# Kernel tuning notes

Hardware: AMD Instinct MI355X
Metric: run time of the kernel (lower is better)

## Reference

```python
import jax, jax.numpy as jnp
from jax import lax
import numpy as np


def _lstm_layer(x, Wih, Whh, bih, bhh):
    """Single-direction LSTM layer, PyTorch gate order (i, f, g, o).
    x: [B, T, D_in] -> hidden sequence [B, T, H]."""
    B, T, _ = x.shape
    H = Whh.shape[1]
    # Precompute input contribution for all timesteps: [B, T, 4H]
    xw = jnp.einsum('btd,gd->btg', x, Wih) + bih + bhh

    def step(carry, xt):
        h, c = carry
        gates = xt + h @ Whh.T  # [B, 4H]
        i, f, g, o = jnp.split(gates, 4, axis=-1)
        i = jax.nn.sigmoid(i)
        f = jax.nn.sigmoid(f)
        g = jnp.tanh(g)
        o = jax.nn.sigmoid(o)
        c = f * c + i * g
        h = o * jnp.tanh(c)
        return (h, c), h

    h0 = jnp.zeros((B, H), dtype=x.dtype)
    c0 = jnp.zeros((B, H), dtype=x.dtype)
    _, hs = lax.scan(step, (h0, c0), jnp.swapaxes(xw, 0, 1))  # [T, B, H]
    return jnp.swapaxes(hs, 0, 1)  # [B, T, H]


def setup_inputs() -> dict:
    key = jax.random.key(0)
    ks = jax.random.split(key, 9)
    B, T, D, H = 64, 2048, 256, 128
    s = 1.0 / np.sqrt(H)  # PyTorch uniform(-1/sqrt(H), 1/sqrt(H)) init scale
    u = lambda k, shp: jax.random.uniform(k, shp, jnp.float32, -s, s)
    return {
        'x': jax.random.normal(ks[0], (B, T, D), jnp.float32),
        'Wih0': u(ks[1], (4 * H, D)),
        'Whh0': u(ks[2], (4 * H, H)),
        'bih0': u(ks[3], (4 * H,)),
        'bhh0': u(ks[4], (4 * H,)),
        'Wih1': u(ks[5], (4 * H, H)),
        'Whh1': u(ks[6], (4 * H, H)),
        'bih1': u(ks[7], (4 * H,)),
        'bhh1': u(ks[8], (4 * H,)),
    }


def reference(x, Wih0, Whh0, bih0, bhh0, Wih1, Whh1, bih1, bhh1):
    # 2-layer stacked LSTM; inter-layer dropout (p=0.1) is identity at eval.
    h1 = _lstm_layer(x, Wih0, Whh0, bih0, bhh0)
    h2 = _lstm_layer(h1, Wih1, Whh1, bih1, bhh1)
    return h2
```

## Files before the change

kernel.cpp:

```cpp
#include <hip/hip_runtime.h>
#include <hip/hip_bf16.h>

#define H 128
#define FOURH 512
#define BATCH 64
#define SEQ 2048
#define TC SEQ
#define NCHUNK 128
#define GSTRIDE (BATCH * FOURH)

typedef _Float16 half8 __attribute__((ext_vector_type(8)));
typedef float f32x4 __attribute__((ext_vector_type(4)));

__global__ void prep_kernel(const float* __restrict__ Wih0,
                            const float* __restrict__ bih0, const float* __restrict__ bhh0,
                            const float* __restrict__ bih1, const float* __restrict__ bhh1,
                            const float* __restrict__ Wih1,
                            float* __restrict__ Wt0,
                            float* __restrict__ b0, float* __restrict__ b1,
                            _Float16* __restrict__ wt1h,
                            int* __restrict__ flags) {
    int id = blockIdx.x * 256 + threadIdx.x;
    const int N0 = 256 * 512;
    if (id < N0) {
        int k = id >> 9, n = id & 511;
        Wt0[id] = Wih0[n * 256 + k];
    } else if (id < N0 + 512) {
        int i = id - N0;
        b0[i] = bih0[i] + bhh0[i];
    } else if (id < N0 + 1024) {
        int i = id - (N0 + 512);
        b1[i] = bih1[i] + bhh1[i];
    } else if (id < N0 + 1024 + 65536) {
        int i = id - (N0 + 1024);
        wt1h[i] = (_Float16)Wih1[i];
    } else if (id < N0 + 1024 + 65536 + 272) {
        flags[id - (N0 + 1024 + 65536)] = 0;
    }
}

__device__ __forceinline__ float sigmoid_f(float x) {
    return __builtin_amdgcn_rcpf(1.f + __expf(-x));
}
__device__ __forceinline__ float tanh_f(float x) {
    return 1.f - 2.f * __builtin_amdgcn_rcpf(__expf(2.f * x) + 1.f);
}

#define LDS_BARRIER()                                                \
    do {                                                             \
        asm volatile("s_waitcnt lgkmcnt(0)" ::: "memory");           \
        __builtin_amdgcn_s_barrier();                                \
        __builtin_amdgcn_sched_barrier(0);                           \
    } while (0)

#define BM 128
#define BN 128
#define BK 32

__global__ __launch_bounds__(512, 2) void lstm_fused_kernel(
    const float* __restrict__ x,
    const float* __restrict__ Wt0,
    const float* __restrict__ b0sum,
    float* __restrict__ Gbuf,
    const float* __restrict__ Whh0,
    const _Float16* __restrict__ wt1h,
    const float* __restrict__ Whh1,
    const float* __restrict__ b1,
    _Float16* __restrict__ h1p,
    float* __restrict__ out,
    int* __restrict__ flags)
{
    const int tid = threadIdx.x;

    int* prodF     = flags;
    int* chunkDone = flags + 16;
    int* g1Done    = flags + 144;

    __shared__ _Float16 hbuf[2][8][136];
    __shared__ float As[BK][BM + 4];
    __shared__ float Bs[BK][BN];

    if (blockIdx.x >= 176) {
        const int j   = blockIdx.x - 176;
        const int sub = j & 31;
        const int cls = j >> 5;
        const int by  = sub >> 2;
        const int bx  = sub & 3;
        const int n0  = bx * BN;
        const int wv  = tid >> 6;
        const int l   = tid & 63;
        const int li  = l & 15;
        const int q   = l >> 4;
        const int gb1 = 8 * by + wv;

        float bv1g[8];
#pragma unroll
        for (int ct = 0; ct < 8; ++ct) bv1g[ct] = b1[n0 + ct * 16 + li];

        for (int m = cls; m < NCHUNK; m += 2) {
            if (tid == 0) {
                while (__hip_atomic_load(&prodF[by], __ATOMIC_RELAXED,
                                         __HIP_MEMORY_SCOPE_AGENT) < 16 * (m + 1))
                    __builtin_amdgcn_s_sleep(4);
                (void)__hip_atomic_load(&prodF[by], __ATOMIC_ACQUIRE,
                                        __HIP_MEMORY_SCOPE_AGENT);
            }
            __syncthreads();

            const int t0 = m * 16;
            half8 Af[4];
            const _Float16* ap = h1p + ((size_t)(t0 + li) * BATCH + gb1) * H + q * 8;
#pragma unroll
            for (int kf = 0; kf < 4; ++kf)
                Af[kf] = *(const half8*)(ap + kf * 32);

            f32x4 acc1[8];
#pragma unroll
            for (int ct = 0; ct < 8; ++ct) {
                acc1[ct][0] = bv1g[ct]; acc1[ct][1] = bv1g[ct];
                acc1[ct][2] = bv1g[ct]; acc1[ct][3] = bv1g[ct];
            }
#pragma unroll
            for (int ct = 0; ct < 8; ++ct) {
                const _Float16* wp = wt1h + (size_t)(n0 + ct * 16 + li) * H + q * 8;
#pragma unroll
                for (int kf = 0; kf < 4; ++kf) {
                    half8 Bfr = *(const half8*)(wp + kf * 32);
                    acc1[ct] = __builtin_amdgcn_mfma_f32_16x16x32_f16(Af[kf], Bfr, acc1[ct], 0, 0, 0);
                }
            }
            const int srow = t0 + q * 4;
#pragma unroll
            for (int ct = 0; ct < 8; ++ct)
#pragma unroll
                for (int i = 0; i < 4; ++i)
                    Gbuf[((size_t)(srow + i) * BATCH + gb1) * FOURH + n0 + ct * 16 + li] = acc1[ct][i];
            __syncthreads();
            if (tid == 0) {
                __threadfence();
                __hip_atomic_fetch_add(&g1Done[m], 1, __ATOMIC_RELEASE,
                                       __HIP_MEMORY_SCOPE_AGENT);
            }
        }
        return;
    }

    if (blockIdx.x >= 16) {
        const int j   = blockIdx.x - 16;
        const int sub = j & 31;
        const int cls = j >> 5;
        const int by  = sub >> 2;
        const int bx  = sub & 3;
        const int n0  = bx * BN;
        const int tm  = tid >> 5;
        const int tn  = tid & 31;

        int ar[2], aq[2], bkk[2], bq[2];
#pragma unroll
        for (int l2 = 0; l2 < 2; ++l2) {
            int fidx = tid + l2 * 512;
            ar[l2] = fidx >> 3; aq[l2] = fidx & 7;
            bkk[l2] = fidx >> 5; bq[l2] = fidx & 31;
        }
        float4 bvg = *(const float4*)&b0sum[n0 + tn * 4];

        for (int idx = cls; idx < NCHUNK; idx += 5) {
            const float* aptr[2];
#pragma unroll
            for (int l2 = 0; l2 < 2; ++l2) {
                int rl = by * BM + ar[l2];
                int b = rl >> 4;
                int t = idx * 16 + (rl & 15);
                aptr[l2] = x + ((size_t)b * SEQ + t) * 256 + aq[l2] * 4;
            }
            float acc[2][4][4];
#pragma unroll
            for (int rh = 0; rh < 2; ++rh)
#pragma unroll
                for (int i = 0; i < 4; ++i)
#pragma unroll
                    for (int jj = 0; jj < 4; ++jj) acc[rh][i][jj] = 0.f;

            for (int k0 = 0; k0 < 256; k0 += BK) {
                __syncthreads();
#pragma unroll
                for (int l2 = 0; l2 < 2; ++l2) {
                    float4 v = *(const float4*)(aptr[l2] + k0);
                    As[aq[l2] * 4 + 0][ar[l2]] = v.x;
                    As[aq[l2] * 4 + 1][ar[l2]] = v.y;
                    As[aq[l2] * 4 + 2][ar[l2]] = v.z;
                    As[aq[l2] * 4 + 3][ar[l2]] = v.w;
                }
#pragma unroll
                for (int l2 = 0; l2 < 2; ++l2) {
                    float4 v = *(const float4*)(Wt0 + (size_t)(k0 + bkk[l2]) * FOURH + n0 + bq[l2] * 4);
                    *(float4*)&Bs[bkk[l2]][bq[l2] * 4] = v;
                }
                __syncthreads();
#pragma unroll
                for (int kk = 0; kk < BK; ++kk) {
                    float a[8], bb[4];
                    *(float4*)&a[0] = *(const float4*)&As[kk][tm * 4];
                    *(float4*)&a[4] = *(const float4*)&As[kk][64 + tm * 4];
                    *(float4*)&bb[0] = *(const float4*)&Bs[kk][tn * 4];
#pragma unroll
                    for (int rh = 0; rh < 2; ++rh)
#pragma unroll
                        for (int i = 0; i < 4; ++i)
#pragma unroll
                            for (int jj = 0; jj < 4; ++jj)
                                acc[rh][i][jj] = fmaf(a[rh * 4 + i], bb[jj], acc[rh][i][jj]);
                }
            }
#pragma unroll
            for (int rh = 0; rh < 2; ++rh)
#pragma unroll
                for (int i = 0; i < 4; ++i) {
                    int rl = by * BM + rh * 64 + tm * 4 + i;
                    int b = rl >> 4;
                    int t = idx * 16 + (rl & 15);
                    float* gp = Gbuf + ((size_t)t * BATCH + b) * FOURH + n0 + tn * 4;
                    float4 o = make_float4(acc[rh][i][0] + bvg.x, acc[rh][i][1] + bvg.y,
                                           acc[rh][i][2] + bvg.z, acc[rh][i][3] + bvg.w);
                    *(float4*)gp = o;
                }
            __syncthreads();
            if (tid == 0) {
                __threadfence();
                __hip_atomic_fetch_add(&chunkDone[idx], 1, __ATOMIC_RELEASE,
                                       __HIP_MEMORY_SCOPE_AGENT);
            }
        }
        return;
    }

    const int w  = tid >> 6;
    const int l  = tid & 63;
    const int li = l & 15;
    const int q  = l >> 4;
    const int u  = 16 * w + li;
    const int b0 = q * 2;
    const int ab = ((li >> 2) * 2) + (li & 1);

#define WAIT_FLAG(ptr, tgtv)                                                   \
    do {                                                                       \
        if (tid == 0) {                                                        \
            while (__hip_atomic_load((ptr), __ATOMIC_RELAXED,                  \
                                     __HIP_MEMORY_SCOPE_AGENT) < (tgtv))       \
                __builtin_amdgcn_s_sleep(4);                                   \
            (void)__hip_atomic_load((ptr), __ATOMIC_ACQUIRE,                   \
                                    __HIP_MEMORY_SCOPE_AGENT);                 \
        }                                                                      \
        __syncthreads();                                                       \
    } while (0)

#define SCAN_STEP(S, PB, GR, BFARR, STORE_STMT)                                   \
    {                                                                             \
        half8 Afr[4];                                                             \
        _Pragma("unroll")                                                         \
        for (int kf = 0; kf < 4; ++kf)                                            \
            Afr[kf] = *(const half8*)&hbuf[PB][ab][kf * 32 + q * 8];              \
        f32x4 acc[4];                                                             \
        _Pragma("unroll")                                                         \
        for (int tl = 0; tl < 4; ++tl) {                                          \
            acc[tl][0] = GR[tl * 2 + 0]; acc[tl][1] = GR[tl * 2 + 1];             \
            acc[tl][2] = 0.f;            acc[tl][3] = 0.f;                        \
        }                                                                         \
        {                                                                         \
            int sl_ = (S) + 4; if (sl_ > TC - 1) sl_ = TC - 1;                    \
            const float* gp_ = Gbuf + (size_t)sl_ * GSTRIDE;                      \
            _Pragma("unroll")                                                     \
            for (int tl = 0; tl < 4; ++tl) {                                      \
                GR[tl * 2 + 0] = gp_[boff0 + tl * H];                             \
                GR[tl * 2 + 1] = gp_[boff1 + tl * H];                             \
            }                                                                     \
        }                                                                         \
        _Pragma("unroll")                                                         \
        for (int kf = 0; kf < 4; ++kf)                                            \
            _Pragma("unroll")                                                     \
            for (int tl = 0; tl < 4; ++tl)                                        \
                acc[tl] = __builtin_amdgcn_mfma_f32_16x16x32_f16(Afr[kf], BFARR[tl][kf], acc[tl], 0, 0, 0); \
        {                                                                         \
            float ig = sigmoid_f(acc[0][0]);                                      \
            float fg = sigmoid_f(acc[1][0]);                                      \
            float gg = tanh_f(acc[2][0]);                                         \
            float og = sigmoid_f(acc[3][0]);                                      \
            c0 = fmaf(fg, c0, ig * gg);                                           \
            h0 = og * tanh_f(c0);                                                 \
            float ig1 = sigmoid_f(acc[0][1]);                                     \
            float fg1 = sigmoid_f(acc[1][1]);                                     \
            float gg1 = tanh_f(acc[2][1]);                                        \
            float og1 = sigmoid_f(acc[3][1]);                                     \
            c1 = fmaf(fg1, c1, ig1 * gg1);                                        \
            h1v = og1 * tanh_f(c1);                                               \
        }                                                                         \
        hbuf[PB ^ 1][b0][u]     = (_Float16)h0;                                   \
        hbuf[PB ^ 1][b0 + 1][u] = (_Float16)h1v;                                  \
        STORE_STMT                                                                \
        LDS_BARRIER();                                                            \
    }

    const int g = (blockIdx.x < 8) ? blockIdx.x : blockIdx.x - 8;
    const int boff0 = (8 * g + b0) * FOURH + u;
    const int boff1 = boff0 + FOURH;

    if (blockIdx.x < 8) {
        half8 Bf[4][4];
#pragma unroll
        for (int tl = 0; tl < 4; ++tl)
#pragma unroll
            for (int kf = 0; kf < 4; ++kf) {
                const float* wp = Whh0 + (size_t)(tl * 128 + u) * H + kf * 32 + q * 8;
                float4 v0 = *(const float4*)wp;
                float4 v1 = *(const float4*)(wp + 4);
                half8 b;
                b[0] = (_Float16)v0.x; b[1] = (_Float16)v0.y;
                b[2] = (_Float16)v0.z; b[3] = (_Float16)v0.w;
                b[4] = (_Float16)v1.x; b[5] = (_Float16)v1.y;
                b[6] = (_Float16)v1.z; b[7] = (_Float16)v1.w;
                Bf[tl][kf] = b;
            }

        float c0 = 0.f, c1 = 0.f, h0 = 0.f, h1v = 0.f;
        hbuf[0][b0][u]     = (_Float16)0.f;
        hbuf[0][b0 + 1][u] = (_Float16)0.f;

        WAIT_FLAG(&chunkDone[0], 32);

        float Ga[8], Gb[8], Gc[8], Gd[8];
#pragma unroll
        for (int tl = 0; tl < 4; ++tl) {
            Ga[tl * 2 + 0] = Gbuf[(size_t)0 * GSTRIDE + boff0 + tl * H];
            Ga[tl * 2 + 1] = Gbuf[(size_t)0 * GSTRIDE + boff1 + tl * H];
            Gb[tl * 2 + 0] = Gbuf[(size_t)1 * GSTRIDE + boff0 + tl * H];
            Gb[tl * 2 + 1] = Gbuf[(size_t)1 * GSTRIDE + boff1 + tl * H];
            Gc[tl * 2 + 0] = Gbuf[(size_t)2 * GSTRIDE + boff0 + tl * H];
            Gc[tl * 2 + 1] = Gbuf[(size_t)2 * GSTRIDE + boff1 + tl * H];
            Gd[tl * 2 + 0] = Gbuf[(size_t)3 * GSTRIDE + boff0 + tl * H];
            Gd[tl * 2 + 1] = Gbuf[(size_t)3 * GSTRIDE + boff1 + tl * H];
        }

        _Float16* php = h1p + (size_t)(8 * g + b0) * H + u;

#define P_STORE { php[0] = (_Float16)h0; php[128] = (_Float16)h1v; php += BATCH * H; }

        for (int s4 = 0; s4 < TC; s4 += 4) {
            if ((s4 & 15) == 0) {
                int k = (s4 >> 4) + 1;
                if (k > NCHUNK - 1) k = NCHUNK - 1;
                WAIT_FLAG(&chunkDone[k], 32);
            }
            SCAN_STEP(s4 + 0, 0, Ga, Bf, P_STORE)
            SCAN_STEP(s4 + 1, 1, Gb, Bf, P_STORE)
            SCAN_STEP(s4 + 2, 0, Gc, Bf, P_STORE)
            SCAN_STEP(s4 + 3, 1, Gd, Bf, P_STORE)
            if ((s4 & 15) == 12) {
                __threadfence();
                __syncthreads();
                if (tid == 0)
                    __hip_atomic_store(&prodF[g], s4 + 4, __ATOMIC_RELEASE,
                                       __HIP_MEMORY_SCOPE_AGENT);
            }
        }
#undef P_STORE
    } else {
        half8 Bf[4][4];
#pragma unroll
        for (int tl = 0; tl < 4; ++tl)
#pragma unroll
            for (int kf = 0; kf < 4; ++kf) {
                const float* wp = Whh1 + (size_t)(tl * 128 + u) * H + kf * 32 + q * 8;
                float4 v0 = *(const float4*)wp;
                float4 v1 = *(const float4*)(wp + 4);
                half8 b;
                b[0] = (_Float16)v0.x; b[1] = (_Float16)v0.y;
                b[2] = (_Float16)v0.z; b[3] = (_Float16)v0.w;
                b[4] = (_Float16)v1.x; b[5] = (_Float16)v1.y;
                b[6] = (_Float16)v1.z; b[7] = (_Float16)v1.w;
                Bf[tl][kf] = b;
            }

        float c0 = 0.f, c1 = 0.f, h0, h1v;
        hbuf[0][b0][u]     = (_Float16)0.f;
        hbuf[0][b0 + 1][u] = (_Float16)0.f;

        float* op0 = out + (size_t)(8 * g + b0) * SEQ * H + u;
        float* op1 = out + (size_t)(8 * g + b0 + 1) * SEQ * H + u;

        WAIT_FLAG(&prodF[g], 96);
        WAIT_FLAG(&g1Done[0], 32);

        float Ga[8], Gb[8], Gc[8], Gd[8];
#pragma unroll
        for (int tl = 0; tl < 4; ++tl) {
            Ga[tl * 2 + 0] = Gbuf[(size_t)0 * GSTRIDE + boff0 + tl * H];
            Ga[tl * 2 + 1] = Gbuf[(size_t)0 * GSTRIDE + boff1 + tl * H];
            Gb[tl * 2 + 0] = Gbuf[(size_t)1 * GSTRIDE + boff0 + tl * H];
            Gb[tl * 2 + 1] = Gbuf[(size_t)1 * GSTRIDE + boff1 + tl * H];
            Gc[tl * 2 + 0] = Gbuf[(size_t)2 * GSTRIDE + boff0 + tl * H];
            Gc[tl * 2 + 1] = Gbuf[(size_t)2 * GSTRIDE + boff1 + tl * H];
            Gd[tl * 2 + 0] = Gbuf[(size_t)3 * GSTRIDE + boff0 + tl * H];
            Gd[tl * 2 + 1] = Gbuf[(size_t)3 * GSTRIDE + boff1 + tl * H];
        }

#define C_STORE { op0[0] = h0; op1[0] = h1v; op0 += H; op1 += H; }

        for (int s4 = 0; s4 < TC; s4 += 4) {
            if ((s4 & 15) == 0) {
                int k = (s4 >> 4) + 1;
                if (k > NCHUNK - 1) k = NCHUNK - 1;
                WAIT_FLAG(&g1Done[k], 32);
            }
            SCAN_STEP(s4 + 0, 0, Ga, Bf, C_STORE)
            SCAN_STEP(s4 + 1, 1, Gb, Bf, C_STORE)
            SCAN_STEP(s4 + 2, 0, Gc, Bf, C_STORE)
            SCAN_STEP(s4 + 3, 1, Gd, Bf, C_STORE)
        }
#undef C_STORE
    }
#undef WAIT_FLAG
#undef SCAN_STEP
}

extern "C" void kernel_launch(void* const* d_in, const int* in_sizes, int n_in,
                              void* d_out, int out_size, void* d_ws, size_t ws_size,
                              hipStream_t stream) {
    const float* x    = (const float*)d_in[0];
    const float* Wih0 = (const float*)d_in[1];
    const float* Whh0 = (const float*)d_in[2];
    const float* bih0 = (const float*)d_in[3];
    const float* bhh0 = (const float*)d_in[4];
    const float* Wih1 = (const float*)d_in[5];
    const float* Whh1 = (const float*)d_in[6];
    const float* bih1 = (const float*)d_in[7];
    const float* bhh1 = (const float*)d_in[8];
    float* out = (float*)d_out;

    char* ws = (char*)d_ws;
    size_t off = 0;
    auto carve = [&](size_t bytes) -> char* {
        char* p = ws + off;
        off += (bytes + 255) & ~(size_t)255;
        return p;
    };

    float*     Wt0   = (float*)carve(256 * 512 * 4);
    float*     b0v   = (float*)carve(512 * 4);
    float*     b1v   = (float*)carve(512 * 4);
    _Float16*  wt1h  = (_Float16*)carve(65536 * 2);
    _Float16*  h1p   = (_Float16*)carve((size_t)SEQ * BATCH * H * 2);
    int*       flags = (int*)carve(272 * 4);
    float*     gbuf  = (float*)carve((size_t)SEQ * GSTRIDE * 4);

    prep_kernel<<<774, 256, 0, stream>>>(Wih0, bih0, bhh0, bih1, bhh1, Wih1,
                                         Wt0, b0v, b1v, wt1h, flags);

    lstm_fused_kernel<<<240, 512, 0, stream>>>(x, Wt0, b0v, gbuf,
                                               Whh0, wt1h, Whh1, b1v,
                                               h1p, out, flags);
}
```

Before: 2.498 ms.

## Move layer-0 input projection GEMM into a separate kernel before fused scan

Layer-0's input-projection GEMM no longer runs inside the persistent fused kernel as 160 producer blocks. It now runs as a standalone tiled FP32 GEMM kernel with bias, launched before the fused LSTM kernel, which shrinks to 80 blocks. The chunkDone flag waits in the layer-0 scan are dropped, so that scan reads precomputed gates directly. This removes the flag polling and the LDS/register pressure the GEMM blocks added to the persistent kernel. In exchange, the GEMM no longer overlaps with the serial recurrence, so its full time is added before the scan starts.

```diff
diff --git a/kernel.cpp b/kernel.cpp
--- a/kernel.cpp
+++ b/kernel.cpp
@@ -39,6 +39,108 @@
     }
 }
 
+#define BM 128
+#define BN 128
+#define BK 32
+
+__global__ __launch_bounds__(256) void gemm_bias_kernel(
+    const float* __restrict__ A, int lda, int rowsPerBatch, int t0,
+    const float* __restrict__ Bt, const float* __restrict__ bias,
+    float* __restrict__ G, int K, int tcShift)
+{
+    __shared__ float As[BK][BM + 4];
+    __shared__ float Bs[BK][BN];
+
+    const int tid = threadIdx.x;
+    const int m0 = blockIdx.y * BM;
+    const int n0 = blockIdx.x * BN;
+    const int tm = tid >> 4;
+    const int tn = tid & 15;
+    const int tcMask = (1 << tcShift) - 1;
+
+    const float* aptr[4];
+    int ar[4], aq[4];
+#pragma unroll
+    for (int l = 0; l < 4; ++l) {
+        int fidx = tid + l * 256;
+        int r = fidx >> 3, q = fidx & 7;
+        ar[l] = r; aq[l] = q;
+        int m = m0 + r;
+        int bi = m >> tcShift;
+        int tl = m & tcMask;
+        aptr[l] = A + ((size_t)bi * rowsPerBatch + t0 + tl) * lda + q * 4;
+    }
+    int bkk[4], bq[4];
+#pragma unroll
+    for (int l = 0; l < 4; ++l) {
+        int fidx = tid + l * 256;
+        bkk[l] = fidx >> 5; bq[l] = fidx & 31;
+    }
+
+    float acc[2][2][4][4];
+#pragma unroll
+    for (int ri = 0; ri < 2; ++ri)
+#pragma unroll
+        for (int ci = 0; ci < 2; ++ci)
+#pragma unroll
+            for (int i = 0; i < 4; ++i)
+#pragma unroll
+                for (int j = 0; j < 4; ++j) acc[ri][ci][i][j] = 0.f;
+
+    for (int k0 = 0; k0 < K; k0 += BK) {
+        __syncthreads();
+#pragma unroll
+        for (int l = 0; l < 4; ++l) {
+            float4 v = *(const float4*)(aptr[l] + k0);
+            As[aq[l] * 4 + 0][ar[l]] = v.x;
+            As[aq[l] * 4 + 1][ar[l]] = v.y;
+            As[aq[l] * 4 + 2][ar[l]] = v.z;
+            As[aq[l] * 4 + 3][ar[l]] = v.w;
+        }
+#pragma unroll
+        for (int l = 0; l < 4; ++l) {
+            float4 v = *(const float4*)(Bt + (size_t)(k0 + bkk[l]) * FOURH + n0 + bq[l] * 4);
+            *(float4*)&Bs[bkk[l]][bq[l] * 4] = v;
+        }
+        __syncthreads();
+#pragma unroll
+        for (int kk = 0; kk < BK; ++kk) {
+            float a[8], bb[8];
+            *(float4*)&a[0] = *(const float4*)&As[kk][tm * 4];
+            *(float4*)&a[4] = *(const float4*)&As[kk][64 + tm * 4];
+            *(float4*)&bb[0] = *(const float4*)&Bs[kk][tn * 4];
+            *(float4*)&bb[4] = *(const float4*)&Bs[kk][64 + tn * 4];
+#pragma unroll
+            for (int ri = 0; ri < 2; ++ri)
+#pragma unroll
+                for (int i = 0; i < 4; ++i)
+#pragma unroll
+                    for (int ci = 0; ci < 2; ++ci)
+#pragma unroll
+                        for (int j = 0; j < 4; ++j)
+                            acc[ri][ci][i][j] = fmaf(a[ri * 4 + i], bb[ci * 4 + j], acc[ri][ci][i][j]);
+        }
+    }
+
+    float4 bv0 = *(const float4*)&bias[n0 + tn * 4];
+    float4 bv1 = *(const float4*)&bias[n0 + 64 + tn * 4];
+#pragma unroll
+    for (int ri = 0; ri < 2; ++ri)
+#pragma unroll
+        for (int i = 0; i < 4; ++i) {
+            int m = m0 + ri * 64 + tm * 4 + i;
+            int bi = m >> tcShift;
+            int tl = m & tcMask;
+            float* gp = G + ((size_t)tl * BATCH + bi) * FOURH + n0;
+            float4 o0 = make_float4(acc[ri][0][i][0] + bv0.x, acc[ri][0][i][1] + bv0.y,
+                                    acc[ri][0][i][2] + bv0.z, acc[ri][0][i][3] + bv0.w);
+            float4 o1 = make_float4(acc[ri][1][i][0] + bv1.x, acc[ri][1][i][1] + bv1.y,
+                                    acc[ri][1][i][2] + bv1.z, acc[ri][1][i][3] + bv1.w);
+            *(float4*)(gp + tn * 4) = o0;
+            *(float4*)(gp + 64 + tn * 4) = o1;
+        }
+}
+
 __device__ __forceinline__ float sigmoid_f(float x) {
     return __builtin_amdgcn_rcpf(1.f + __expf(-x));
 }
@@ -53,14 +155,7 @@
         __builtin_amdgcn_sched_barrier(0);                           \
     } while (0)
 
-#define BM 128
-#define BN 128
-#define BK 32
-
 __global__ __launch_bounds__(512, 2) void lstm_fused_kernel(
-    const float* __restrict__ x,
-    const float* __restrict__ Wt0,
-    const float* __restrict__ b0sum,
     float* __restrict__ Gbuf,
     const float* __restrict__ Whh0,
     const _Float16* __restrict__ wt1h,
@@ -72,21 +167,18 @@
 {
     const int tid = threadIdx.x;
 
-    int* prodF     = flags;
-    int* chunkDone = flags + 16;
-    int* g1Done    = flags + 144;
+    int* prodF  = flags;
+    int* g1Done = flags + 144;
 
     __shared__ _Float16 hbuf[2][8][136];
-    __shared__ float As[BK][BM + 4];
-    __shared__ float Bs[BK][BN];
-
-    if (blockIdx.x >= 176) {
-        const int j   = blockIdx.x - 176;
+
+    if (blockIdx.x >= 16) {
+        const int j   = blockIdx.x - 16;
         const int sub = j & 31;
         const int cls = j >> 5;
         const int by  = sub >> 2;
         const int bx  = sub & 3;
-        const int n0  = bx * BN;
+        const int n0  = bx * 128;
         const int wv  = tid >> 6;
         const int l   = tid & 63;
         const int li  = l & 15;
@@ -139,95 +231,6 @@
             if (tid == 0) {
                 __threadfence();
                 __hip_atomic_fetch_add(&g1Done[m], 1, __ATOMIC_RELEASE,
-                                       __HIP_MEMORY_SCOPE_AGENT);
-            }
-        }
-        return;
-    }
-
-    if (blockIdx.x >= 16) {
-        const int j   = blockIdx.x - 16;
-        const int sub = j & 31;
-        const int cls = j >> 5;
-        const int by  = sub >> 2;
-        const int bx  = sub & 3;
-        const int n0  = bx * BN;
-        const int tm  = tid >> 5;
-        const int tn  = tid & 31;
-
-        int ar[2], aq[2], bkk[2], bq[2];
-#pragma unroll
-        for (int l2 = 0; l2 < 2; ++l2) {
-            int fidx = tid + l2 * 512;
-            ar[l2] = fidx >> 3; aq[l2] = fidx & 7;
-            bkk[l2] = fidx >> 5; bq[l2] = fidx & 31;
-        }
-        float4 bvg = *(const float4*)&b0sum[n0 + tn * 4];
-
-        for (int idx = cls; idx < NCHUNK; idx += 5) {
-            const float* aptr[2];
-#pragma unroll
-            for (int l2 = 0; l2 < 2; ++l2) {
-                int rl = by * BM + ar[l2];
-                int b = rl >> 4;
-                int t = idx * 16 + (rl & 15);
-                aptr[l2] = x + ((size_t)b * SEQ + t) * 256 + aq[l2] * 4;
-            }
-            float acc[2][4][4];
-#pragma unroll
-            for (int rh = 0; rh < 2; ++rh)
-#pragma unroll
-                for (int i = 0; i < 4; ++i)
-#pragma unroll
-                    for (int jj = 0; jj < 4; ++jj) acc[rh][i][jj] = 0.f;
-
-            for (int k0 = 0; k0 < 256; k0 += BK) {
-                __syncthreads();
-#pragma unroll
-                for (int l2 = 0; l2 < 2; ++l2) {
-                    float4 v = *(const float4*)(aptr[l2] + k0);
-                    As[aq[l2] * 4 + 0][ar[l2]] = v.x;
-                    As[aq[l2] * 4 + 1][ar[l2]] = v.y;
-                    As[aq[l2] * 4 + 2][ar[l2]] = v.z;
-                    As[aq[l2] * 4 + 3][ar[l2]] = v.w;
-                }
-#pragma unroll
-                for (int l2 = 0; l2 < 2; ++l2) {
-                    float4 v = *(const float4*)(Wt0 + (size_t)(k0 + bkk[l2]) * FOURH + n0 + bq[l2] * 4);
-                    *(float4*)&Bs[bkk[l2]][bq[l2] * 4] = v;
-                }
-                __syncthreads();
-#pragma unroll
-                for (int kk = 0; kk < BK; ++kk) {
-                    float a[8], bb[4];
-                    *(float4*)&a[0] = *(const float4*)&As[kk][tm * 4];
-                    *(float4*)&a[4] = *(const float4*)&As[kk][64 + tm * 4];
-                    *(float4*)&bb[0] = *(const float4*)&Bs[kk][tn * 4];
-#pragma unroll
-                    for (int rh = 0; rh < 2; ++rh)
-#pragma unroll
-                        for (int i = 0; i < 4; ++i)
-#pragma unroll
-                            for (int jj = 0; jj < 4; ++jj)
-                                acc[rh][i][jj] = fmaf(a[rh * 4 + i], bb[jj], acc[rh][i][jj]);
-                }
-            }
-#pragma unroll
-            for (int rh = 0; rh < 2; ++rh)
-#pragma unroll
-                for (int i = 0; i < 4; ++i) {
-                    int rl = by * BM + rh * 64 + tm * 4 + i;
-                    int b = rl >> 4;
-                    int t = idx * 16 + (rl & 15);
-                    float* gp = Gbuf + ((size_t)t * BATCH + b) * FOURH + n0 + tn * 4;
-                    float4 o = make_float4(acc[rh][i][0] + bvg.x, acc[rh][i][1] + bvg.y,
-                                           acc[rh][i][2] + bvg.z, acc[rh][i][3] + bvg.w);
-                    *(float4*)gp = o;
-                }
-            __syncthreads();
-            if (tid == 0) {
-                __threadfence();
-                __hip_atomic_fetch_add(&chunkDone[idx], 1, __ATOMIC_RELEASE,
                                        __HIP_MEMORY_SCOPE_AGENT);
             }
         }
@@ -324,8 +327,7 @@
         float c0 = 0.f, c1 = 0.f, h0 = 0.f, h1v = 0.f;
         hbuf[0][b0][u]     = (_Float16)0.f;
         hbuf[0][b0 + 1][u] = (_Float16)0.f;
-
-        WAIT_FLAG(&chunkDone[0], 32);
+        __syncthreads();
 
         float Ga[8], Gb[8], Gc[8], Gd[8];
 #pragma unroll
@@ -345,11 +347,6 @@
 #define P_STORE { php[0] = (_Float16)h0; php[128] = (_Float16)h1v; php += BATCH * H; }
 
         for (int s4 = 0; s4 < TC; s4 += 4) {
-            if ((s4 & 15) == 0) {
-                int k = (s4 >> 4) + 1;
-                if (k > NCHUNK - 1) k = NCHUNK - 1;
-                WAIT_FLAG(&chunkDone[k], 32);
-            }
             SCAN_STEP(s4 + 0, 0, Ga, Bf, P_STORE)
             SCAN_STEP(s4 + 1, 1, Gb, Bf, P_STORE)
             SCAN_STEP(s4 + 2, 0, Gc, Bf, P_STORE)
@@ -455,7 +452,9 @@
     prep_kernel<<<774, 256, 0, stream>>>(Wih0, bih0, bhh0, bih1, bhh1, Wih1,
                                          Wt0, b0v, b1v, wt1h, flags);
 
-    lstm_fused_kernel<<<240, 512, 0, stream>>>(x, Wt0, b0v, gbuf,
-                                               Whh0, wt1h, Whh1, b1v,
-                                               h1p, out, flags);
-}
+    dim3 ggrid(FOURH / BN, (BATCH * SEQ) / BM);
+    gemm_bias_kernel<<<ggrid, 256, 0, stream>>>(x, 256, SEQ, 0, Wt0, b0v, gbuf, 256, 11);
+
+    lstm_fused_kernel<<<80, 512, 0, stream>>>(gbuf, Whh0, wt1h, Whh1, b1v,
+                                              h1p, out, flags);
+}
```

Result: faster. 2.361 ms (-5.5%).
